# Kernel optimization log

Measured on AMD Instinct MI355X. Metric: run time of the kernel, lower is better.

## Reference

```python
import jax, jax.numpy as jnp
import numpy as np

N_NODES = 100000
N_EDGES = 3200000
IN_CH = 128
OUT_CH = 64


def gcn_conv(x, src, dst, W, b, n):
    """PyG GCNConv: out = D^{-1/2} (A+I) D^{-1/2} (x @ W) + b.
    src/dst already include self-loops. Aggregation at dst (source_to_target)."""
    deg = jax.ops.segment_sum(jnp.ones_like(dst, x.dtype), dst, num_segments=n)  # [N]
    dinv = jnp.where(deg > 0, jax.lax.rsqrt(deg), 0.0)
    norm = dinv[src] * dinv[dst]                     # [E+N]
    xw = x @ W                                       # [N, out] dense GEMM first (PyG order)
    msgs = xw[src] * norm[:, None]                   # gather + scale, [E+N, out]
    return jax.ops.segment_sum(msgs, dst, num_segments=n) + b


def setup_inputs() -> dict:
    key = jax.random.key(0)
    ks = jax.random.split(key, 6)
    x = jax.random.normal(ks[0], (N_NODES, IN_CH), dtype=jnp.float32)
    edge_index = jax.random.randint(ks[1], (2, N_EDGES), 0, N_NODES, dtype=jnp.int32)
    # Glorot-style init for GCNConv weights
    W1 = jax.random.normal(ks[2], (IN_CH, IN_CH), dtype=jnp.float32) * (1.0 / np.sqrt(IN_CH))
    b1 = jnp.zeros((IN_CH,), dtype=jnp.float32)
    W2 = jax.random.normal(ks[3], (IN_CH, OUT_CH), dtype=jnp.float32) * (1.0 / np.sqrt(IN_CH))
    b2 = jnp.zeros((OUT_CH,), dtype=jnp.float32)
    return {"x": x, "edge_index": edge_index, "W1": W1, "b1": b1, "W2": W2, "b2": b2}


def reference(x, edge_index, W1, b1, W2, b2):
    n = x.shape[0]
    loop = jnp.arange(n, dtype=edge_index.dtype)
    src = jnp.concatenate([edge_index[0], loop])  # add self-loops once; reused by both layers
    dst = jnp.concatenate([edge_index[1], loop])
    h = jax.nn.sigmoid(gcn_conv(x, src, dst, W1, b1, n))
    return jax.nn.sigmoid(gcn_conv(h, src, dst, W2, b2, n))
```

## Files before the change

kernel.cpp:

```cpp
#include <hip/hip_runtime.h>
#include <hip/hip_bf16.h>
#include <hip/hip_fp16.h>

#define IN_CH 128
#define NODES_PER_BUCKET 128
#define BUCKET_CAP 5120
#define EDGES_PER_BLOCK 16384

using f32x2 = __attribute__((ext_vector_type(2))) float;

__device__ __forceinline__ float sigmoidf_(float x) { return 1.0f / (1.0f + __expf(-x)); }
__device__ __forceinline__ __half2 u2h(unsigned u) { return __builtin_bit_cast(__half2, u); }
__device__ __forceinline__ unsigned packh2(float a, float b) {
    return __builtin_bit_cast(unsigned, __float22half2_rn(make_float2(a, b)));
}

#if __has_builtin(__builtin_amdgcn_cvt_pk_f32_fp8) && __has_builtin(__builtin_amdgcn_cvt_pk_fp8_f32)
#define FP8_HW 1
#else
#define FP8_HW 0
__device__ __forceinline__ unsigned fp8_enc1(float f) {
    unsigned short us = __builtin_bit_cast(unsigned short, __float2half(f));
    unsigned s = (us >> 8) & 0x80u;
    unsigned mag = us & 0x7fffu;
    if (mag < 0x2400u) return s;
    unsigned t = mag - 0x2000u;
    t += 0x3Fu + ((t >> 7) & 1u);
    unsigned r = t >> 7;
    if (r > 0x7Eu) r = 0x7Eu;
    return s | r;
}
__device__ __forceinline__ float fp8_dec1(unsigned v) {
    unsigned s = (v & 0x80u) << 8;
    unsigned m = v & 0x7Fu;
    unsigned h = m ? (((m << 7) + 0x2000u) | s) : s;
    return __half2float(__builtin_bit_cast(__half, (unsigned short)h));
}
#endif

__device__ __forceinline__ void acc16(float* a, uint4 v) {
#if FP8_HW
    f32x2 t;
    t = __builtin_amdgcn_cvt_pk_f32_fp8(v.x, false); a[0] += t[0];  a[1] += t[1];
    t = __builtin_amdgcn_cvt_pk_f32_fp8(v.x, true);  a[2] += t[0];  a[3] += t[1];
    t = __builtin_amdgcn_cvt_pk_f32_fp8(v.y, false); a[4] += t[0];  a[5] += t[1];
    t = __builtin_amdgcn_cvt_pk_f32_fp8(v.y, true);  a[6] += t[0];  a[7] += t[1];
    t = __builtin_amdgcn_cvt_pk_f32_fp8(v.z, false); a[8] += t[0];  a[9] += t[1];
    t = __builtin_amdgcn_cvt_pk_f32_fp8(v.z, true);  a[10] += t[0]; a[11] += t[1];
    t = __builtin_amdgcn_cvt_pk_f32_fp8(v.w, false); a[12] += t[0]; a[13] += t[1];
    t = __builtin_amdgcn_cvt_pk_f32_fp8(v.w, true);  a[14] += t[0]; a[15] += t[1];
#else
    unsigned d[4] = {v.x, v.y, v.z, v.w};
#pragma unroll
    for (int q = 0; q < 4; q++)
#pragma unroll
        for (int b = 0; b < 4; b++) a[q * 4 + b] += fp8_dec1((d[q] >> (8 * b)) & 0xffu);
#endif
}

__device__ __forceinline__ unsigned pack4fp8(float a, float b, float c, float d) {
#if FP8_HW
    unsigned r = 0;
    r = __builtin_amdgcn_cvt_pk_fp8_f32(a, b, r, false);
    r = __builtin_amdgcn_cvt_pk_fp8_f32(c, d, r, true);
    return r;
#else
    return fp8_enc1(a) | (fp8_enc1(b) << 8) | (fp8_enc1(c) << 16) | (fp8_enc1(d) << 24);
#endif
}

__global__ __launch_bounds__(256) void k_bucket_scatter(const int* __restrict__ src,
                                                        const int* __restrict__ dst, int E,
                                                        int* __restrict__ bucketCnt, int NB,
                                                        unsigned* __restrict__ pairBuf) {
    __shared__ int hist[1024];
    for (int t = threadIdx.x; t < NB; t += 256) hist[t] = 0;
    __syncthreads();
    int base = blockIdx.x * EDGES_PER_BLOCK;
    int end = min(base + EDGES_PER_BLOCK, E);
    for (int idx = base + threadIdx.x; idx < end; idx += 256)
        atomicAdd(&hist[dst[idx] >> 7], 1);
    __syncthreads();
    for (int t = threadIdx.x; t < NB; t += 256) {
        int c = hist[t];
        hist[t] = c ? atomicAdd(&bucketCnt[t], c) : 0;
    }
    __syncthreads();
    for (int idx = base + threadIdx.x; idx < end; idx += 256) {
        int d = dst[idx];
        int b = d >> 7;
        int pos = atomicAdd(&hist[b], 1);
        if (pos < BUCKET_CAP)
            pairBuf[(size_t)b * BUCKET_CAP + pos] = ((unsigned)src[idx] << 7) | (unsigned)(d & 127);
    }
}

__global__ __launch_bounds__(1024) void k_scan_buckets(const int* __restrict__ bucketCnt, int NB,
                                                       int* __restrict__ bucketBase,
                                                       int* __restrict__ rowptr, int n) {
    __shared__ int sh[1024];
    int t = threadIdx.x;
    int v = (t < NB) ? min(bucketCnt[t], BUCKET_CAP) : 0;
    sh[t] = v;
    __syncthreads();
    for (int off = 1; off < 1024; off <<= 1) {
        int u = (t >= off) ? sh[t - off] : 0;
        __syncthreads();
        sh[t] += u;
        __syncthreads();
    }
    if (t < NB) bucketBase[t] = sh[t] - v;
    if (t == 1023) rowptr[n] = sh[1023];
}

__global__ __launch_bounds__(256) void k_bucket_place2(const unsigned* __restrict__ pairBuf,
                                                       const int* __restrict__ bucketCnt,
                                                       const int* __restrict__ bucketBase,
                                                       int* __restrict__ rowptr,
                                                       float* __restrict__ dinv,
                                                       int* __restrict__ col, int n) {
    __shared__ int hist[NODES_PER_BUCKET];
    __shared__ int excl[NODES_PER_BUCKET];
    __shared__ int stage[BUCKET_CAP];
    int b = blockIdx.x;
    int tid = threadIdx.x;
    int first = b * NODES_PER_BUCKET;
    if (tid < NODES_PER_BUCKET) hist[tid] = 0;
    __syncthreads();
    int cb = min(bucketCnt[b], BUCKET_CAP);
    const unsigned* p = pairBuf + (size_t)b * BUCKET_CAP;
    for (int e = tid; e < cb; e += 256) atomicAdd(&hist[p[e] & 127], 1);
    __syncthreads();
    int v = (tid < NODES_PER_BUCKET) ? hist[tid] : 0;
    if (tid < NODES_PER_BUCKET) excl[tid] = v;
    __syncthreads();
    for (int off = 1; off < NODES_PER_BUCKET; off <<= 1) {
        int u = (tid < NODES_PER_BUCKET && tid >= off) ? excl[tid - off] : 0;
        __syncthreads();
        if (tid < NODES_PER_BUCKET) excl[tid] += u;
        __syncthreads();
    }
    int base = bucketBase[b];
    if (tid < NODES_PER_BUCKET) {
        int node = first + tid;
        int ex = excl[tid] - v;
        if (node < n) {
            rowptr[node] = base + ex;
            dinv[node] = rsqrtf((float)(v + 1));
        }
        hist[tid] = ex;
    }
    __syncthreads();
    for (int e = tid; e < cb; e += 256) {
        unsigned pr = p[e];
        int lpos = atomicAdd(&hist[pr & 127], 1);
        stage[lpos] = (int)(pr >> 7);
    }
    __syncthreads();
    for (int i = tid; i < cb; i += 256) col[base + i] = stage[i];
}

template <int OUTC, bool INHALF>
__global__ __launch_bounds__(256) void k_gemm_scale(const void* __restrict__ Xv,
                                                    const float* __restrict__ W,
                                                    const float* __restrict__ dinv,
                                                    unsigned char* __restrict__ Yb, int n) {
    constexpr int TN = OUTC / 16;
    __shared__ float xs[16][65];
    __shared__ float ws[16 * OUTC];
    int tid = threadIdx.x;
    int row0 = blockIdx.x * 64;
    int tx = tid & 15;
    int ty = tid >> 4;

    float acc[4][TN];
#pragma unroll
    for (int i = 0; i < 4; i++)
#pragma unroll
        for (int j = 0; j < TN; j++) acc[i][j] = 0.0f;

    for (int k0 = 0; k0 < IN_CH; k0 += 16) {
        {
            int r = tid >> 2;
            int kq = (tid & 3) * 4;
            int grow = row0 + r;
            float4 xv = make_float4(0.f, 0.f, 0.f, 0.f);
            if (grow < n) {
                if constexpr (INHALF) {
                    uint2 xu = *(const uint2*)((const unsigned short*)Xv + (size_t)grow * IN_CH + k0 + kq);
                    __half2 p0 = u2h(xu.x), p1 = u2h(xu.y);
                    xv = make_float4(__low2float(p0), __high2float(p0), __low2float(p1), __high2float(p1));
                } else {
                    xv = *(const float4*)((const float*)Xv + (size_t)grow * IN_CH + k0 + kq);
                }
            }
            xs[kq + 0][r] = xv.x;
            xs[kq + 1][r] = xv.y;
            xs[kq + 2][r] = xv.z;
            xs[kq + 3][r] = xv.w;
        }
        {
            const float4* wsrc = (const float4*)(W + k0 * OUTC);
            float4* wdst = (float4*)ws;
#pragma unroll
            for (int j = 0; j < OUTC / 64; j++) wdst[tid + j * 256] = wsrc[tid + j * 256];
        }
        __syncthreads();
#pragma unroll
        for (int kk = 0; kk < 16; kk++) {
            float a[4];
            *(float4*)a = *(const float4*)&xs[kk][ty * 4];
            float bb[TN];
#pragma unroll
            for (int j = 0; j < TN / 4; j++)
                *(float4*)&bb[j * 4] = *(const float4*)&ws[kk * OUTC + tx * TN + j * 4];
#pragma unroll
            for (int i = 0; i < 4; i++)
#pragma unroll
                for (int j = 0; j < TN; j++) acc[i][j] = fmaf(a[i], bb[j], acc[i][j]);
        }
        __syncthreads();
    }
#pragma unroll
    for (int i = 0; i < 4; i++) {
        int grow = row0 + ty * 4 + i;
        if (grow < n) {
            float dvv = dinv[grow];
            if constexpr (TN == 8) {
                uint2 o;
                o.x = pack4fp8(acc[i][0] * dvv, acc[i][1] * dvv, acc[i][2] * dvv, acc[i][3] * dvv);
                o.y = pack4fp8(acc[i][4] * dvv, acc[i][5] * dvv, acc[i][6] * dvv, acc[i][7] * dvv);
                ((uint2*)(Yb + (size_t)grow * 128))[tx] = o;
            } else {
                unsigned o = pack4fp8(acc[i][0] * dvv, acc[i][1] * dvv, acc[i][2] * dvv, acc[i][3] * dvv);
                ((unsigned*)(Yb + (size_t)grow * 64))[tx] = o;
            }
        }
    }
}

template <int C, bool OUTHALF>
__global__ __launch_bounds__(256) void k_agg(const uint4* __restrict__ Y4,
                                             const int* __restrict__ rowptr,
                                             const int* __restrict__ col,
                                             const float* __restrict__ dinv,
                                             const float* __restrict__ bias,
                                             void* __restrict__ out, int n, int zidx) {
    constexpr int LPE = C / 16;
    constexpr int EPI = 16 / LPE;
    constexpr int RS = C / 16;
    int gid = blockIdx.x * blockDim.x + threadIdx.x;
    int wid = gid >> 6;
    int lane = gid & 63;
    int node = wid * 4 + (lane >> 4);
    if (node >= n) return;
    int hl = lane & 15;
    int g = hl / LPE;
    int sub = hl % LPE;
    int s0 = rowptr[node], s1 = rowptr[node + 1];

    float a0[16], a1[16];
#pragma unroll
    for (int k = 0; k < 16; k++) { a0[k] = 0.f; a1[k] = 0.f; }

    {
        int idx = (g == 0) ? node : zidx;
        uint4 v = Y4[(size_t)idx * RS + sub];
        acc16(a0, v);
    }
    int i = s0;
    for (; i + 2 * EPI <= s1; i += 2 * EPI) {
        int ca = col[i + g];
        int cb = col[i + EPI + g];
        uint4 va = Y4[(size_t)ca * RS + sub];
        uint4 vb = Y4[(size_t)cb * RS + sub];
        acc16(a0, va);
        acc16(a1, vb);
    }
    for (; i < s1; i += EPI) {
        int e = i + g;
        int c = col[min(e, s1 - 1)];
        int idx = (e < s1) ? c : zidx;
        uint4 v = Y4[(size_t)idx * RS + sub];
        acc16(a0, v);
    }
#pragma unroll
    for (int k = 0; k < 16; k++) a0[k] += a1[k];
#pragma unroll
    for (int m = LPE; m < 16; m <<= 1) {
#pragma unroll
        for (int k = 0; k < 16; k++) a0[k] += __shfl_xor(a0[k], m, 64);
    }
    if (hl < LPE) {
        float dv = dinv[node];
        float4 bv[4];
        bv[0] = *(const float4*)&bias[sub * 16];
        bv[1] = *(const float4*)&bias[sub * 16 + 4];
        bv[2] = *(const float4*)&bias[sub * 16 + 8];
        bv[3] = *(const float4*)&bias[sub * 16 + 12];
        float o[16];
#pragma unroll
        for (int q = 0; q < 4; q++) {
            const float* bq = (const float*)&bv[q];
#pragma unroll
            for (int b = 0; b < 4; b++) o[q * 4 + b] = sigmoidf_(a0[q * 4 + b] * dv + bq[b]);
        }
        if constexpr (OUTHALF) {
            constexpr int OR = C / 8;
            uint4 h0, h1;
            h0.x = packh2(o[0], o[1]);   h0.y = packh2(o[2], o[3]);
            h0.z = packh2(o[4], o[5]);   h0.w = packh2(o[6], o[7]);
            h1.x = packh2(o[8], o[9]);   h1.y = packh2(o[10], o[11]);
            h1.z = packh2(o[12], o[13]); h1.w = packh2(o[14], o[15]);
            ((uint4*)out)[(size_t)node * OR + sub * 2] = h0;
            ((uint4*)out)[(size_t)node * OR + sub * 2 + 1] = h1;
        } else {
            float* op = (float*)out + (size_t)node * C + sub * 16;
            *(float4*)(op + 0)  = make_float4(o[0], o[1], o[2], o[3]);
            *(float4*)(op + 4)  = make_float4(o[4], o[5], o[6], o[7]);
            *(float4*)(op + 8)  = make_float4(o[8], o[9], o[10], o[11]);
            *(float4*)(op + 12) = make_float4(o[12], o[13], o[14], o[15]);
        }
    }
}

extern "C" void kernel_launch(void* const* d_in, const int* in_sizes, int n_in,
                              void* d_out, int out_size, void* d_ws, size_t ws_size,
                              hipStream_t stream) {
    const float* x  = (const float*)d_in[0];
    const int* eidx = (const int*)d_in[1];
    const float* W1 = (const float*)d_in[2];
    const float* b1 = (const float*)d_in[3];
    const float* W2 = (const float*)d_in[4];
    const float* b2 = (const float*)d_in[5];
    float* out = (float*)d_out;

    int n = in_sizes[0] / IN_CH;
    int E = in_sizes[1] / 2;
    const int* srcv = eidx;
    const int* dstv = eidx + E;
    int NB = (n + NODES_PER_BUCKET - 1) / NODES_PER_BUCKET;

    char* w = (char*)d_ws;
    auto alloc = [&](size_t bytes) {
        char* p = w;
        w += (bytes + 255) & ~(size_t)255;
        return p;
    };
    int* bucketCnt      = (int*)alloc((size_t)NB * 4);
    int* bucketBase     = (int*)alloc((size_t)NB * 4);
    unsigned* pairBuf   = (unsigned*)alloc((size_t)NB * BUCKET_CAP * 4);
    int* rowptr         = (int*)alloc(((size_t)n + 1) * 4);
    float* dinv         = (float*)alloc((size_t)n * 4);
    int* col            = (int*)alloc((size_t)E * 4);
    unsigned char* y    = (unsigned char*)alloc(((size_t)n + 1) * 128);
    unsigned short* h   = (unsigned short*)alloc((size_t)n * IN_CH * 2);

    hipMemsetAsync(bucketCnt, 0, (size_t)NB * 4, stream);
    hipMemsetAsync(y + (size_t)n * 128, 0, 128, stream);
    int nblk = (E + EDGES_PER_BLOCK - 1) / EDGES_PER_BLOCK;
    k_bucket_scatter<<<nblk, 256, 0, stream>>>(srcv, dstv, E, bucketCnt, NB, pairBuf);
    k_scan_buckets<<<1, 1024, 0, stream>>>(bucketCnt, NB, bucketBase, rowptr, n);
    k_bucket_place2<<<NB, 256, 0, stream>>>(pairBuf, bucketCnt, bucketBase, rowptr, dinv, col, n);

    int gemmGrid = (n + 63) / 64;
    int aggGrid = (n + 15) / 16;

    k_gemm_scale<128, false><<<gemmGrid, 256, 0, stream>>>(x, W1, dinv, y, n);
    k_agg<128, true><<<aggGrid, 256, 0, stream>>>((const uint4*)y, rowptr, col, dinv, b1, h, n, n);
    k_gemm_scale<64, true><<<gemmGrid, 256, 0, stream>>>(h, W2, dinv, y, n);
    k_agg<64, false><<<aggGrid, 256, 0, stream>>>((const uint4*)y, rowptr, col, dinv, b2, out, n, 2 * n);
}
```

Baseline: 277.0 us.

## Scatter edges into per-block segments with local offsets instead of global buckets

The scatter kernel now writes each edge block's pairs into its own contiguous segment, sorted by bucket through a block-local prefix scan, and records per-block bucket offsets. The bucket-based global atomic slot reservation and scattered writes into capacity-sized bucket regions go away. The place kernel then gathers each bucket's pairs by walking all edge blocks' segments through the offset table. This gives coalesced, contention-free scatter writes, but each place block must now read roughly nblk offset pairs and many short fragments, and the offset table adds memory.

```diff
diff --git a/kernel.cpp b/kernel.cpp
--- a/kernel.cpp
+++ b/kernel.cpp
@@ -5,7 +5,7 @@
 #define IN_CH 128
 #define NODES_PER_BUCKET 128
 #define BUCKET_CAP 5120
-#define EDGES_PER_BLOCK 16384
+#define EPB 4096
 
 using f32x2 = __attribute__((ext_vector_type(2))) float;
 
@@ -69,29 +69,54 @@
 #endif
 }
 
-__global__ __launch_bounds__(256) void k_bucket_scatter(const int* __restrict__ src,
-                                                        const int* __restrict__ dst, int E,
-                                                        int* __restrict__ bucketCnt, int NB,
-                                                        unsigned* __restrict__ pairBuf) {
+__global__ __launch_bounds__(256) void k_scatter2(const int* __restrict__ src,
+                                                  const int* __restrict__ dst, int E,
+                                                  int* __restrict__ bucketCnt, int NB,
+                                                  unsigned* __restrict__ pairBuf,
+                                                  int* __restrict__ bbo) {
     __shared__ int hist[1024];
-    for (int t = threadIdx.x; t < NB; t += 256) hist[t] = 0;
-    __syncthreads();
-    int base = blockIdx.x * EDGES_PER_BLOCK;
-    int end = min(base + EDGES_PER_BLOCK, E);
-    for (int idx = base + threadIdx.x; idx < end; idx += 256)
-        atomicAdd(&hist[dst[idx] >> 7], 1);
-    __syncthreads();
-    for (int t = threadIdx.x; t < NB; t += 256) {
-        int c = hist[t];
-        hist[t] = c ? atomicAdd(&bucketCnt[t], c) : 0;
-    }
-    __syncthreads();
-    for (int idx = base + threadIdx.x; idx < end; idx += 256) {
-        int d = dst[idx];
+    __shared__ int part[256];
+    int blk = blockIdx.x;
+    int tid = threadIdx.x;
+    for (int t = tid; t < 1024; t += 256) hist[t] = 0;
+    __syncthreads();
+    int base = blk * EPB;
+    int end = min(base + EPB, E);
+    for (int i = base + tid; i < end; i += 256)
+        atomicAdd(&hist[dst[i] >> 7], 1);
+    __syncthreads();
+    int b0 = tid * 4;
+    int v[4];
+    int s = 0;
+#pragma unroll
+    for (int j = 0; j < 4; j++) { v[j] = hist[b0 + j]; s += v[j]; }
+    part[tid] = s;
+    __syncthreads();
+    for (int off = 1; off < 256; off <<= 1) {
+        int u = (tid >= off) ? part[tid - off] : 0;
+        __syncthreads();
+        part[tid] += u;
+        __syncthreads();
+    }
+    int run = part[tid] - s;
+    size_t bb = (size_t)blk * NB;
+#pragma unroll
+    for (int j = 0; j < 4; j++) {
+        int b = b0 + j;
+        if (b < NB) {
+            bbo[bb + b] = run;
+            if (v[j]) atomicAdd(&bucketCnt[b], v[j]);
+        }
+        hist[b] = run;
+        run += v[j];
+    }
+    __syncthreads();
+    unsigned* seg = pairBuf + (size_t)blk * EPB;
+    for (int i = base + tid; i < end; i += 256) {
+        int d = dst[i];
         int b = d >> 7;
         int pos = atomicAdd(&hist[b], 1);
-        if (pos < BUCKET_CAP)
-            pairBuf[(size_t)b * BUCKET_CAP + pos] = ((unsigned)src[idx] << 7) | (unsigned)(d & 127);
+        seg[pos] = ((unsigned)src[i] << 7) | (unsigned)(d & 127);
     }
 }
 
@@ -113,12 +138,14 @@
     if (t == 1023) rowptr[n] = sh[1023];
 }
 
-__global__ __launch_bounds__(256) void k_bucket_place2(const unsigned* __restrict__ pairBuf,
-                                                       const int* __restrict__ bucketCnt,
-                                                       const int* __restrict__ bucketBase,
-                                                       int* __restrict__ rowptr,
-                                                       float* __restrict__ dinv,
-                                                       int* __restrict__ col, int n) {
+__global__ __launch_bounds__(256) void k_place2(const unsigned* __restrict__ pairBuf,
+                                                const int* __restrict__ bbo,
+                                                const int* __restrict__ bucketCnt,
+                                                const int* __restrict__ bucketBase,
+                                                int* __restrict__ rowptr,
+                                                float* __restrict__ dinv,
+                                                int* __restrict__ col,
+                                                int n, int NB, int nblk, int E) {
     __shared__ int hist[NODES_PER_BUCKET];
     __shared__ int excl[NODES_PER_BUCKET];
     __shared__ int stage[BUCKET_CAP];
@@ -127,9 +154,15 @@
     int first = b * NODES_PER_BUCKET;
     if (tid < NODES_PER_BUCKET) hist[tid] = 0;
     __syncthreads();
-    int cb = min(bucketCnt[b], BUCKET_CAP);
-    const unsigned* p = pairBuf + (size_t)b * BUCKET_CAP;
-    for (int e = tid; e < cb; e += 256) atomicAdd(&hist[p[e] & 127], 1);
+    int gg = tid >> 4;
+    int gl = tid & 15;
+    for (int blk = gg; blk < nblk; blk += 16) {
+        int off0 = bbo[(size_t)blk * NB + b];
+        int off1 = (b + 1 < NB) ? bbo[(size_t)blk * NB + b + 1] : min(EPB, E - blk * EPB);
+        const unsigned* pp = pairBuf + (size_t)blk * EPB;
+        for (int e = off0 + gl; e < off1; e += 16)
+            atomicAdd(&hist[pp[e] & 127], 1);
+    }
     __syncthreads();
     int v = (tid < NODES_PER_BUCKET) ? hist[tid] : 0;
     if (tid < NODES_PER_BUCKET) excl[tid] = v;
@@ -151,12 +184,18 @@
         hist[tid] = ex;
     }
     __syncthreads();
-    for (int e = tid; e < cb; e += 256) {
-        unsigned pr = p[e];
-        int lpos = atomicAdd(&hist[pr & 127], 1);
-        stage[lpos] = (int)(pr >> 7);
-    }
-    __syncthreads();
+    for (int blk = gg; blk < nblk; blk += 16) {
+        int off0 = bbo[(size_t)blk * NB + b];
+        int off1 = (b + 1 < NB) ? bbo[(size_t)blk * NB + b + 1] : min(EPB, E - blk * EPB);
+        const unsigned* pp = pairBuf + (size_t)blk * EPB;
+        for (int e = off0 + gl; e < off1; e += 16) {
+            unsigned pr = pp[e];
+            int lpos = atomicAdd(&hist[pr & 127], 1);
+            if (lpos < BUCKET_CAP) stage[lpos] = (int)(pr >> 7);
+        }
+    }
+    __syncthreads();
+    int cb = min(bucketCnt[b], BUCKET_CAP);
     for (int i = tid; i < cb; i += 256) col[base + i] = stage[i];
 }
 
@@ -340,6 +379,7 @@
     const int* srcv = eidx;
     const int* dstv = eidx + E;
     int NB = (n + NODES_PER_BUCKET - 1) / NODES_PER_BUCKET;
+    int nblk = (E + EPB - 1) / EPB;
 
     char* w = (char*)d_ws;
     auto alloc = [&](size_t bytes) {
@@ -349,7 +389,8 @@
     };
     int* bucketCnt      = (int*)alloc((size_t)NB * 4);
     int* bucketBase     = (int*)alloc((size_t)NB * 4);
-    unsigned* pairBuf   = (unsigned*)alloc((size_t)NB * BUCKET_CAP * 4);
+    unsigned* pairBuf   = (unsigned*)alloc((size_t)nblk * EPB * 4);
+    int* bbo            = (int*)alloc((size_t)nblk * NB * 4);
     int* rowptr         = (int*)alloc(((size_t)n + 1) * 4);
     float* dinv         = (float*)alloc((size_t)n * 4);
     int* col            = (int*)alloc((size_t)E * 4);
@@ -358,10 +399,11 @@
 
     hipMemsetAsync(bucketCnt, 0, (size_t)NB * 4, stream);
     hipMemsetAsync(y + (size_t)n * 128, 0, 128, stream);
-    int nblk = (E + EDGES_PER_BLOCK - 1) / EDGES_PER_BLOCK;
-    k_bucket_scatter<<<nblk, 256, 0, stream>>>(srcv, dstv, E, bucketCnt, NB, pairBuf);
+
+    k_scatter2<<<nblk, 256, 0, stream>>>(srcv, dstv, E, bucketCnt, NB, pairBuf, bbo);
     k_scan_buckets<<<1, 1024, 0, stream>>>(bucketCnt, NB, bucketBase, rowptr, n);
-    k_bucket_place2<<<NB, 256, 0, stream>>>(pairBuf, bucketCnt, bucketBase, rowptr, dinv, col, n);
+    k_place2<<<NB, 256, 0, stream>>>(pairBuf, bbo, bucketCnt, bucketBase, rowptr, dinv, col,
+                                     n, NB, nblk, E);
 
     int gemmGrid = (n + 63) / 64;
     int aggGrid = (n + 15) / 16;
```

Result: slower. 359.5 us (+29.8%).

## Assign one node per lane group in aggregation and vectorize bucket scatter

Applied to the files above, without the earlier changes.

The aggregation kernel now gives each node only LPE lanes (8 or 4) instead of 16 lanes split into edge groups. Each lane group walks its node's edges serially, which removes the cross-group shuffle reduction and packs 8 or 16 nodes per wavefront. The bucket scatter kernel halves edges per block and reads src/dst as int4 to vectorize the histogram and placement loops. In exchange, per-lane serial edge loops are longer and degree imbalance within a wavefront causes divergence. The int4 loads also assume the src and dst arrays are 16-byte aligned.

```diff
diff --git a/kernel.cpp b/kernel.cpp
--- a/kernel.cpp
+++ b/kernel.cpp
@@ -5,7 +5,7 @@
 #define IN_CH 128
 #define NODES_PER_BUCKET 128
 #define BUCKET_CAP 5120
-#define EDGES_PER_BLOCK 16384
+#define EPB 8192
 
 using f32x2 = __attribute__((ext_vector_type(2))) float;
 
@@ -74,24 +74,47 @@
                                                         int* __restrict__ bucketCnt, int NB,
                                                         unsigned* __restrict__ pairBuf) {
     __shared__ int hist[1024];
-    for (int t = threadIdx.x; t < NB; t += 256) hist[t] = 0;
-    __syncthreads();
-    int base = blockIdx.x * EDGES_PER_BLOCK;
-    int end = min(base + EDGES_PER_BLOCK, E);
-    for (int idx = base + threadIdx.x; idx < end; idx += 256)
-        atomicAdd(&hist[dst[idx] >> 7], 1);
-    __syncthreads();
-    for (int t = threadIdx.x; t < NB; t += 256) {
+    int tid = threadIdx.x;
+    for (int t = tid; t < 1024; t += 256) hist[t] = 0;
+    __syncthreads();
+    int base = blockIdx.x * EPB;
+    int end = min(base + EPB, E);
+    int cnt4 = (end - base) >> 2;
+    const int4* d4 = (const int4*)(dst + base);
+    const int4* s4 = (const int4*)(src + base);
+    for (int i = tid; i < cnt4; i += 256) {
+        int4 d = d4[i];
+        atomicAdd(&hist[d.x >> 7], 1);
+        atomicAdd(&hist[d.y >> 7], 1);
+        atomicAdd(&hist[d.z >> 7], 1);
+        atomicAdd(&hist[d.w >> 7], 1);
+    }
+    for (int i = base + (cnt4 << 2) + tid; i < end; i += 256)
+        atomicAdd(&hist[dst[i] >> 7], 1);
+    __syncthreads();
+    for (int t = tid; t < NB; t += 256) {
         int c = hist[t];
         hist[t] = c ? atomicAdd(&bucketCnt[t], c) : 0;
     }
     __syncthreads();
-    for (int idx = base + threadIdx.x; idx < end; idx += 256) {
-        int d = dst[idx];
+    for (int i = tid; i < cnt4; i += 256) {
+        int4 d = d4[i];
+        int4 s = s4[i];
+        int b, p;
+        b = d.x >> 7; p = atomicAdd(&hist[b], 1);
+        if (p < BUCKET_CAP) pairBuf[(size_t)b * BUCKET_CAP + p] = ((unsigned)s.x << 7) | (unsigned)(d.x & 127);
+        b = d.y >> 7; p = atomicAdd(&hist[b], 1);
+        if (p < BUCKET_CAP) pairBuf[(size_t)b * BUCKET_CAP + p] = ((unsigned)s.y << 7) | (unsigned)(d.y & 127);
+        b = d.z >> 7; p = atomicAdd(&hist[b], 1);
+        if (p < BUCKET_CAP) pairBuf[(size_t)b * BUCKET_CAP + p] = ((unsigned)s.z << 7) | (unsigned)(d.z & 127);
+        b = d.w >> 7; p = atomicAdd(&hist[b], 1);
+        if (p < BUCKET_CAP) pairBuf[(size_t)b * BUCKET_CAP + p] = ((unsigned)s.w << 7) | (unsigned)(d.w & 127);
+    }
+    for (int i = base + (cnt4 << 2) + tid; i < end; i += 256) {
+        int d = dst[i];
         int b = d >> 7;
-        int pos = atomicAdd(&hist[b], 1);
-        if (pos < BUCKET_CAP)
-            pairBuf[(size_t)b * BUCKET_CAP + pos] = ((unsigned)src[idx] << 7) | (unsigned)(d & 127);
+        int p = atomicAdd(&hist[b], 1);
+        if (p < BUCKET_CAP) pairBuf[(size_t)b * BUCKET_CAP + p] = ((unsigned)src[i] << 7) | (unsigned)(d & 127);
     }
 }
 
@@ -247,51 +270,45 @@
                                              const float* __restrict__ bias,
                                              void* __restrict__ out, int n, int zidx) {
     constexpr int LPE = C / 16;
-    constexpr int EPI = 16 / LPE;
+    constexpr int NPW = 64 / LPE;
     constexpr int RS = C / 16;
     int gid = blockIdx.x * blockDim.x + threadIdx.x;
     int wid = gid >> 6;
     int lane = gid & 63;
-    int node = wid * 4 + (lane >> 4);
-    if (node >= n) return;
-    int hl = lane & 15;
-    int g = hl / LPE;
-    int sub = hl % LPE;
-    int s0 = rowptr[node], s1 = rowptr[node + 1];
+    int g = lane / LPE;
+    int sub = lane % LPE;
+    int node = wid * NPW + g;
+    bool valid = node < n;
+    int nc = valid ? node : 0;
+    int s0 = rowptr[nc];
+    int s1 = valid ? rowptr[nc + 1] : s0;
 
     float a0[16], a1[16];
 #pragma unroll
     for (int k = 0; k < 16; k++) { a0[k] = 0.f; a1[k] = 0.f; }
 
     {
-        int idx = (g == 0) ? node : zidx;
+        int idx = valid ? node : zidx;
         uint4 v = Y4[(size_t)idx * RS + sub];
         acc16(a0, v);
     }
-    int i = s0;
-    for (; i + 2 * EPI <= s1; i += 2 * EPI) {
-        int ca = col[i + g];
-        int cb = col[i + EPI + g];
+    int e = s0;
+    for (; e + 2 <= s1; e += 2) {
+        int ca = col[e];
+        int cb = col[e + 1];
         uint4 va = Y4[(size_t)ca * RS + sub];
         uint4 vb = Y4[(size_t)cb * RS + sub];
         acc16(a0, va);
         acc16(a1, vb);
     }
-    for (; i < s1; i += EPI) {
-        int e = i + g;
-        int c = col[min(e, s1 - 1)];
-        int idx = (e < s1) ? c : zidx;
-        uint4 v = Y4[(size_t)idx * RS + sub];
+    if (e < s1) {
+        uint4 v = Y4[(size_t)col[e] * RS + sub];
         acc16(a0, v);
     }
 #pragma unroll
     for (int k = 0; k < 16; k++) a0[k] += a1[k];
-#pragma unroll
-    for (int m = LPE; m < 16; m <<= 1) {
-#pragma unroll
-        for (int k = 0; k < 16; k++) a0[k] += __shfl_xor(a0[k], m, 64);
-    }
-    if (hl < LPE) {
+
+    if (valid) {
         float dv = dinv[node];
         float4 bv[4];
         bv[0] = *(const float4*)&bias[sub * 16];
@@ -358,16 +375,16 @@
 
     hipMemsetAsync(bucketCnt, 0, (size_t)NB * 4, stream);
     hipMemsetAsync(y + (size_t)n * 128, 0, 128, stream);
-    int nblk = (E + EDGES_PER_BLOCK - 1) / EDGES_PER_BLOCK;
+
+    int nblk = (E + EPB - 1) / EPB;
     k_bucket_scatter<<<nblk, 256, 0, stream>>>(srcv, dstv, E, bucketCnt, NB, pairBuf);
     k_scan_buckets<<<1, 1024, 0, stream>>>(bucketCnt, NB, bucketBase, rowptr, n);
     k_bucket_place2<<<NB, 256, 0, stream>>>(pairBuf, bucketCnt, bucketBase, rowptr, dinv, col, n);
 
     int gemmGrid = (n + 63) / 64;
-    int aggGrid = (n + 15) / 16;
 
     k_gemm_scale<128, false><<<gemmGrid, 256, 0, stream>>>(x, W1, dinv, y, n);
-    k_agg<128, true><<<aggGrid, 256, 0, stream>>>((const uint4*)y, rowptr, col, dinv, b1, h, n, n);
+    k_agg<128, true><<<(n + 31) / 32, 256, 0, stream>>>((const uint4*)y, rowptr, col, dinv, b1, h, n, n);
     k_gemm_scale<64, true><<<gemmGrid, 256, 0, stream>>>(h, W2, dinv, y, n);
-    k_agg<64, false><<<aggGrid, 256, 0, stream>>>((const uint4*)y, rowptr, col, dinv, b2, out, n, 2 * n);
-}
+    k_agg<64, false><<<(n + 63) / 64, 256, 0, stream>>>((const uint4*)y, rowptr, col, dinv, b2, out, n, 2 * n);
+}
```

After: 279.2 us. About the same (+0.8%).
